# Performance work log

Measured on AMD Instinct MI355X. Metric: run time of the kernel, lower is better.

Reference implementation:

```python
import jax, jax.numpy as jnp
import numpy as np

Q_HEADS = 16
KV_HEADS = 4
ROPE_THETA = 10000.0


def _rope(x, seq_len):
    # x: [B, S, H, D]; pairs are consecutive along D (view_as_complex semantics)
    D = x.shape[-1]
    inv_freq = 1.0 / (ROPE_THETA ** (jnp.arange(0, D, 2, dtype=jnp.float32) / D))
    freqs = jnp.arange(seq_len, dtype=jnp.float32)[:, None] * inv_freq  # [S, D/2]
    cos = jnp.cos(freqs)[None, :, None, :]
    sin = jnp.sin(freqs)[None, :, None, :]
    xr = x.reshape(x.shape[:-1] + (D // 2, 2))
    x0, x1 = xr[..., 0], xr[..., 1]
    out = jnp.stack([x0 * cos - x1 * sin, x0 * sin + x1 * cos], axis=-1)
    return out.reshape(x.shape)


def setup_inputs() -> dict:
    key = jax.random.key(0)
    ks = jax.random.split(key, 6)
    B, S, E = 1, 2048, 2048
    KV_DIM = KV_HEADS * (E // Q_HEADS)  # 512
    scale = 0.02
    return {
        "x": jax.random.normal(ks[0], (B, S, E), dtype=jnp.float32),
        "Wq": jax.random.normal(ks[1], (E, E), dtype=jnp.float32) * scale,
        "Wk": jax.random.normal(ks[2], (KV_DIM, E), dtype=jnp.float32) * scale,
        "Wv": jax.random.normal(ks[3], (KV_DIM, E), dtype=jnp.float32) * scale,
        "Wo": jax.random.normal(ks[4], (E, E), dtype=jnp.float32) * scale,
        "bo": jax.random.normal(ks[5], (E,), dtype=jnp.float32) * scale,
        "cache_keys": jnp.zeros((B, S, KV_HEADS, E // Q_HEADS), dtype=jnp.float32),
        "cache_value": jnp.zeros((B, S, KV_HEADS, E // Q_HEADS), dtype=jnp.float32),
        "start_pos": 0,
    }


def reference(x, Wq, Wk, Wv, Wo, bo, cache_keys, cache_value, start_pos):
    B, S, E = x.shape
    hd = E // Q_HEADS
    G = Q_HEADS // KV_HEADS  # queries per kv head

    xq = (x @ Wq.T).reshape(B, S, Q_HEADS, hd)
    xk = (x @ Wk.T).reshape(B, S, KV_HEADS, hd)
    xv = (x @ Wv.T).reshape(B, S, KV_HEADS, hd)

    # Original applies RoPE with positions 0..seq_len-1 for both q and k
    # (freq tensor is sliced [:seq_len] inside apply_rotry_position_embedding).
    xq = _rope(xq, S)
    xk = _rope(xk, S)

    # cache write at start_pos (static python int)
    cache_keys = jax.lax.dynamic_update_slice(cache_keys, xk, (0, start_pos, 0, 0))
    cache_value = jax.lax.dynamic_update_slice(cache_value, xv, (0, start_pos, 0, 0))
    total = start_pos + S
    k_full = cache_keys[:, :total]   # [B, T, KVH, hd]
    v_full = cache_value[:, :total]

    # repeat_interleave over the head axis == GQA expansion
    k = jnp.repeat(k_full, G, axis=2)  # [B, T, QH, hd]
    v = jnp.repeat(v_full, G, axis=2)

    scores = jnp.einsum("bshd,bthd->bhst", xq, k) / jnp.sqrt(jnp.float32(hd))
    causal = jnp.triu(jnp.ones((S, total), dtype=bool), k=1)  # [S, T]
    scores = jnp.where(causal[None, None, :, :], -jnp.inf, scores)
    weights = jax.nn.softmax(scores, axis=-1)
    out = jnp.einsum("bhst,bthd->bshd", weights, v).reshape(B, S, E)
    # dropout p=0.0 / eval mode -> identity
    return out @ Wo.T + bo
```

## Files before the change

kernel.cpp:

```cpp
#include <hip/hip_runtime.h>
#include <stdint.h>

typedef unsigned short u16;
typedef float  f32x4  __attribute__((ext_vector_type(4)));
typedef __bf16 bf16x8 __attribute__((ext_vector_type(8)));
typedef __bf16 bf16x4 __attribute__((ext_vector_type(4)));
typedef unsigned short u16x8 __attribute__((ext_vector_type(8)));
typedef unsigned short u16x4v __attribute__((ext_vector_type(4)));

#define S_LEN 2048
#define E_DIM 2048
#define HD    128
#define QH    16
#define KVH   4
#define KVD   512
#define NQKV  3072
#define QK_SCALE 0.08838834764831845f

#define AS1 __attribute__((address_space(1)))
#define AS3 __attribute__((address_space(3)))

__device__ __forceinline__ u16 f2bf(float f) {
  union { float f; uint32_t u; } v; v.f = f;
  return (u16)((v.u + 0x7FFFu + ((v.u >> 16) & 1u)) >> 16);
}

__global__ void cast_bf16_kernel(const float* __restrict__ in, u16* __restrict__ out) {
  int i = blockIdx.x * blockDim.x + threadIdx.x;
  float4 f = reinterpret_cast<const float4*>(in)[i];
  u16x4v o;
  o[0] = f2bf(f.x); o[1] = f2bf(f.y); o[2] = f2bf(f.z); o[3] = f2bf(f.w);
  reinterpret_cast<u16x4v*>(out)[i] = o;
}

template<bool BIAS>
__global__ __launch_bounds__(256) void gemm_bt_kernel(
    const u16* __restrict__ A, const u16* __restrict__ B,
    float* __restrict__ C, const float* __restrict__ bias,
    int M, int N, int K)
{
  __shared__ u16 As[2][128 * 64];
  __shared__ u16 Bs[2][128 * 64];

  const int tid  = threadIdx.x;
  const int lane = tid & 63;
  const int wid  = tid >> 6;
  const int wr   = (wid >> 1) * 64;
  const int wc   = (wid & 1) * 64;
  const int lr   = lane & 15;
  const int kg   = lane >> 4;

  const int bm = blockIdx.y * 128;
  const int bn = blockIdx.x * 128;

  f32x4 acc[4][4];
  #pragma unroll
  for (int r = 0; r < 4; ++r)
    #pragma unroll
    for (int c = 0; c < 4; ++c) acc[r][c] = (f32x4){0.f, 0.f, 0.f, 0.f};

  const int l8 = lane & 7;
  const int l3 = lane >> 3;
  const int schunk = l8 ^ l3;

  const u16* gA = A + (size_t)(bm + wid*32 + l3) * K + schunk * 8;
  const u16* gB = B + (size_t)(bn + wid*32 + l3) * K + schunk * 8;

  const int sw = lr & 7;

  auto stage = [&](int buf, int kt) {
    #pragma unroll
    for (int i = 0; i < 4; ++i) {
      __builtin_amdgcn_global_load_lds(
          (const AS1 void*)(gA + (size_t)i * 8 * K + kt),
          (AS3 void*)(&As[buf][wid*32*64 + i*8*64]), 16, 0, 0);
      __builtin_amdgcn_global_load_lds(
          (const AS1 void*)(gB + (size_t)i * 8 * K + kt),
          (AS3 void*)(&Bs[buf][wid*32*64 + i*8*64]), 16, 0, 0);
    }
  };

  stage(0, 0);
  __syncthreads();

  int cur = 0;
  for (int kt = 0; kt < K; kt += 64) {
    if (kt + 64 < K) stage(cur ^ 1, kt + 64);
    #pragma unroll
    for (int kk = 0; kk < 2; ++kk) {
      bf16x8 af[4], bfr[4];
      #pragma unroll
      for (int r = 0; r < 4; ++r)
        af[r] = *reinterpret_cast<const bf16x8*>(
            &As[cur][(wr + r*16 + lr)*64 + ((kk*4 + kg) ^ sw)*8]);
      #pragma unroll
      for (int c = 0; c < 4; ++c)
        bfr[c] = *reinterpret_cast<const bf16x8*>(
            &Bs[cur][(wc + c*16 + lr)*64 + ((kk*4 + kg) ^ sw)*8]);
      #pragma unroll
      for (int r = 0; r < 4; ++r)
        #pragma unroll
        for (int c = 0; c < 4; ++c)
          acc[r][c] = __builtin_amdgcn_mfma_f32_16x16x32_bf16(af[r], bfr[c], acc[r][c], 0, 0, 0);
    }
    __syncthreads();
    cur ^= 1;
  }

  const int crow = kg * 4;
  #pragma unroll
  for (int r = 0; r < 4; ++r) {
    #pragma unroll
    for (int c = 0; c < 4; ++c) {
      int gr = bm + wr + r*16 + crow;
      int gc = bn + wc + c*16 + lr;
      float badd = BIAS ? bias[gc] : 0.0f;
      #pragma unroll
      for (int reg = 0; reg < 4; ++reg)
        C[(size_t)(gr + reg)*N + gc] = acc[r][c][reg] + badd;
    }
  }
}

__global__ void rope_split_kernel(const float* __restrict__ qkv,
                                  u16* __restrict__ qb, u16* __restrict__ kb) {
  int idx = blockIdx.x * blockDim.x + threadIdx.x;
  int s  = idx / 1280;
  int cp = idx - s * 1280;
  int col = cp * 2;
  const float* src = qkv + (size_t)s * NQKV + col;
  float x0 = src[0], x1 = src[1];
  int p = (col & 127) >> 1;
  float inv = exp2f((float)p * (-13.287712379549449f / 64.0f));
  float ang = (float)s * inv;
  float sn, cs;
  sincosf(ang, &sn, &cs);
  float o0 = x0 * cs - x1 * sn;
  float o1 = x0 * sn + x1 * cs;
  if (col < E_DIM) {
    o0 *= QK_SCALE; o1 *= QK_SCALE;
    qb[(size_t)s * E_DIM + col]     = f2bf(o0);
    qb[(size_t)s * E_DIM + col + 1] = f2bf(o1);
  } else {
    kb[(size_t)s * KVD + (col - E_DIM)]     = f2bf(o0);
    kb[(size_t)s * KVD + (col - E_DIM) + 1] = f2bf(o1);
  }
}

__global__ void transpose_v_kernel(const float* __restrict__ qkv, u16* __restrict__ vT) {
  __shared__ float tile[32][33];
  const int sbase = blockIdx.x * 32;
  const int cbase = blockIdx.y * 32;
  const int tx = threadIdx.x;
  const int ty = threadIdx.y;
  #pragma unroll
  for (int i = 0; i < 32; i += 8)
    tile[ty + i][tx] = qkv[(size_t)(sbase + ty + i) * NQKV + (E_DIM + KVD) + cbase + tx];
  __syncthreads();
  #pragma unroll
  for (int i = 0; i < 32; i += 8)
    vT[(size_t)(cbase + ty + i) * S_LEN + sbase + tx] = f2bf(tile[tx][ty + i]);
}

__device__ __forceinline__ void attn_tile(
    int t, int qt, int wid, int lr, int kg,
    const bf16x8* qf, f32x4* o, float& mr, float& ls,
    const u16* ks, const u16* vts, u16* ps)
{
  const int sw = lr & 7;
  f32x4 st[4];
  #pragma unroll
  for (int c = 0; c < 4; ++c) st[c] = (f32x4){0.f, 0.f, 0.f, 0.f};
  __builtin_amdgcn_s_setprio(1);
  #pragma unroll
  for (int kk = 0; kk < 4; ++kk) {
    #pragma unroll
    for (int c = 0; c < 4; ++c) {
      bf16x8 kfr = *reinterpret_cast<const bf16x8*>(
          &ks[(c*16 + lr)*128 + ((kk*4 + kg) ^ sw)*8]);
      st[c] = __builtin_amdgcn_mfma_f32_16x16x32_bf16(kfr, qf[kk], st[c], 0, 0, 0);
    }
  }
  __builtin_amdgcn_s_setprio(0);
  if (t == qt) {
    #pragma unroll
    for (int c = 0; c < 4; ++c)
      #pragma unroll
      for (int reg = 0; reg < 4; ++reg)
        if (c*16 + kg*4 + reg > wid*16 + lr) st[c][reg] = -1e30f;
  }
  float cm[4];
  #pragma unroll
  for (int c = 0; c < 4; ++c)
    cm[c] = fmaxf(fmaxf(st[c][0], st[c][1]), fmaxf(st[c][2], st[c][3]));
  float pm = fmaxf(fmaxf(cm[0], cm[1]), fmaxf(cm[2], cm[3]));
  pm = fmaxf(pm, __shfl_xor(pm, 16));
  pm = fmaxf(pm, __shfl_xor(pm, 32));

  if (!__all(pm - mr <= 8.0f)) {
    float nm = fmaxf(mr, pm);
    float alpha = __expf(mr - nm);
    ls *= alpha;
    mr = nm;
    float ar[4];
    #pragma unroll
    for (int reg = 0; reg < 4; ++reg)
      ar[reg] = __shfl(alpha, kg*4 + reg);
    #pragma unroll
    for (int d = 0; d < 8; ++d)
      #pragma unroll
      for (int reg = 0; reg < 4; ++reg)
        o[d][reg] *= ar[reg];
  }

  float p[4][4];
  float csum[4];
  #pragma unroll
  for (int c = 0; c < 4; ++c) {
    #pragma unroll
    for (int reg = 0; reg < 4; ++reg)
      p[c][reg] = __expf(st[c][reg] - mr);
    csum[c] = (p[c][0] + p[c][1]) + (p[c][2] + p[c][3]);
  }
  float sum = (csum[0] + csum[1]) + (csum[2] + csum[3]);
  sum += __shfl_xor(sum, 16);
  sum += __shfl_xor(sum, 32);
  ls += sum;

  #pragma unroll
  for (int c = 0; c < 4; ++c) {
    bf16x4 pk;
    #pragma unroll
    for (int reg = 0; reg < 4; ++reg) pk[reg] = (__bf16)p[c][reg];
    *reinterpret_cast<bf16x4*>(&ps[lr*72 + c*16 + kg*4]) = pk;
  }
  __builtin_amdgcn_s_setprio(1);
  #pragma unroll
  for (int kk = 0; kk < 2; ++kk) {
    bf16x8 pa = *reinterpret_cast<const bf16x8*>(&ps[lr*72 + kk*32 + kg*8]);
    #pragma unroll
    for (int d = 0; d < 8; ++d) {
      bf16x8 vb = *reinterpret_cast<const bf16x8*>(
          &vts[(d*16 + lr)*64 + ((kk*4 + kg) ^ sw)*8]);
      o[d] = __builtin_amdgcn_mfma_f32_16x16x32_bf16(pa, vb, o[d], 0, 0, 0);
    }
  }
  __builtin_amdgcn_s_setprio(0);
}

__global__ __launch_bounds__(256, 2) void attn_kernel(
    const u16* __restrict__ Q, const u16* __restrict__ Kc,
    const u16* __restrict__ VT, u16* __restrict__ Out)
{
  __shared__ u16 Ks[2][64 * 128];
  __shared__ u16 VTs[2][128 * 64];
  __shared__ u16 Ps[4][16 * 72];

  const int x = blockIdx.x;
  int qt, h;
  if (x < 256) { qt = x & 31; h = x >> 5; }
  else         { int xp = x - 256; qt = 31 - (xp & 31); h = 8 + (xp >> 5); }
  const int kvh = h >> 2;
  const int tid  = threadIdx.x;
  const int lane = tid & 63;
  const int wid  = tid >> 6;
  const int lr   = lane & 15;
  const int kg   = lane >> 4;

  const int NT = qt + 1;

  bf16x8 qf[4];
  {
    const u16* qa = Q + (size_t)(qt*64 + wid*16 + lr) * E_DIM + h * HD + kg * 8;
    #pragma unroll
    for (int kk = 0; kk < 4; ++kk)
      qf[kk] = *reinterpret_cast<const bf16x8*>(qa + kk * 32);
  }

  f32x4 o[8];
  #pragma unroll
  for (int d = 0; d < 8; ++d) o[d] = (f32x4){0.f,0.f,0.f,0.f};
  float mr = -1e30f, ls = 0.f;

  u16x8 kreg[4], vreg[4];
  const u16* kbase = Kc + kvh * HD;
  const u16* vbase = VT + (size_t)(kvh * HD) * S_LEN;

  auto stage_load = [&](int t) {
    #pragma unroll
    for (int i = 0; i < 4; ++i) {
      int c = i * 256 + tid;
      kreg[i] = *reinterpret_cast<const u16x8*>(
          kbase + (size_t)(t*64 + (c >> 4)) * KVD + (c & 15) * 8);
      vreg[i] = *reinterpret_cast<const u16x8*>(
          vbase + (size_t)(c >> 3) * S_LEN + t*64 + (c & 7) * 8);
    }
  };
  auto stage_write = [&](int b) {
    #pragma unroll
    for (int i = 0; i < 4; ++i) {
      int c = i * 256 + tid;
      int kr = c >> 4, kc = c & 15;
      *reinterpret_cast<u16x8*>(&Ks[b][kr*128 + (kc ^ (kr & 7))*8]) = kreg[i];
      int vr = c >> 3, vc = c & 7;
      *reinterpret_cast<u16x8*>(&VTs[b][vr*64 + (vc ^ (vr & 7))*8]) = vreg[i];
    }
  };

  int p = 0;
  stage_load(0);
  stage_write(0);
  __syncthreads();

  for (int t = 0; t < NT; ++t) {
    if (t + 1 < NT) stage_load(t + 1);
    attn_tile(t, qt, wid, lr, kg, qf, o, mr, ls, Ks[p], VTs[p], Ps[wid]);
    if (t + 1 < NT) {
      stage_write(p ^ 1);
      __syncthreads();
      p ^= 1;
    }
  }

  {
    float inv = 1.0f / ls;
    float ivq[4];
    #pragma unroll
    for (int reg = 0; reg < 4; ++reg)
      ivq[reg] = __shfl(inv, kg*4 + reg);
    #pragma unroll
    for (int reg = 0; reg < 4; ++reg) {
      int grow = qt*64 + wid*16 + kg*4 + reg;
      #pragma unroll
      for (int d = 0; d < 8; ++d)
        Out[(size_t)grow * E_DIM + h * HD + d*16 + lr] =
            __builtin_bit_cast(u16, (__bf16)(o[d][reg] * ivq[reg]));
    }
  }
}

extern "C" void kernel_launch(void* const* d_in, const int* in_sizes, int n_in,
                              void* d_out, int out_size, void* d_ws, size_t ws_size,
                              hipStream_t stream)
{
  const float* x  = (const float*)d_in[0];
  const float* Wq = (const float*)d_in[1];
  const float* Wk = (const float*)d_in[2];
  const float* Wv = (const float*)d_in[3];
  const float* Wo = (const float*)d_in[4];
  const float* bo = (const float*)d_in[5];
  float* out = (float*)d_out;

  char* w = (char*)d_ws;
  u16*   xb   = (u16*)(w);
  u16*   Wcat = (u16*)(w + (8u  << 20));
  u16*   Wob  = (u16*)(w + (20u << 20));
  float* qkv  = (float*)(w + (28u << 20));
  u16*   qb   = (u16*)(w + (52u << 20));
  u16*   kb   = (u16*)(w + (60u << 20));
  u16*   vT   = (u16*)(w + (62u << 20));
  u16*   attn = (u16*)(w + (64u << 20));
  (void)ws_size; (void)in_sizes; (void)n_in; (void)out_size;

  cast_bf16_kernel<<<4096, 256, 0, stream>>>(x,  xb);
  cast_bf16_kernel<<<4096, 256, 0, stream>>>(Wq, Wcat);
  cast_bf16_kernel<<<1024, 256, 0, stream>>>(Wk, Wcat + (size_t)E_DIM * E_DIM);
  cast_bf16_kernel<<<1024, 256, 0, stream>>>(Wv, Wcat + (size_t)(E_DIM + KVD) * E_DIM);
  cast_bf16_kernel<<<4096, 256, 0, stream>>>(Wo, Wob);

  gemm_bt_kernel<false><<<dim3(NQKV/128, S_LEN/128), 256, 0, stream>>>(
      xb, Wcat, qkv, nullptr, S_LEN, NQKV, E_DIM);

  rope_split_kernel<<<(S_LEN * 1280) / 256, 256, 0, stream>>>(qkv, qb, kb);
  transpose_v_kernel<<<dim3(S_LEN/32, KVD/32), dim3(32, 8), 0, stream>>>(qkv, vT);

  attn_kernel<<<512, 256, 0, stream>>>(qb, kb, vT, attn);

  gemm_bt_kernel<true><<<dim3(E_DIM/128, S_LEN/128), 256, 0, stream>>>(
      attn, Wob, out, bo, S_LEN, E_DIM, E_DIM);
}
```

Baseline: 153.6 us.

## Stream V from global directly, DMA K to LDS, raise occupancy

The attention kernel drops the V shared-memory staging and reads V^T fragments straight from global memory into registers for the PV MFMAs. K tiles are now copied with global_load_lds direct-to-LDS DMA, which removes the register round trip and the separate LDS write step. The swizzle moves to the source address. Freeing LDS lets the launch bound go from 2 to 3 blocks per CU, and the block-to-(qt,h) mapping is reshuffled to pair short and long causal rows. The risk is that V global reads sit on the critical path with higher latency, and that there are more redundant L2 reads across the four q-heads sharing each KV head.

```diff
diff --git a/kernel.cpp b/kernel.cpp
--- a/kernel.cpp
+++ b/kernel.cpp
@@ -165,7 +165,7 @@
 __device__ __forceinline__ void attn_tile(
     int t, int qt, int wid, int lr, int kg,
     const bf16x8* qf, f32x4* o, float& mr, float& ls,
-    const u16* ks, const u16* vts, u16* ps)
+    const u16* ks, const u16* vcol, u16* ps)
 {
   const int sw = lr & 7;
   f32x4 st[4];
@@ -234,33 +234,46 @@
     for (int reg = 0; reg < 4; ++reg) pk[reg] = (__bf16)p[c][reg];
     *reinterpret_cast<bf16x4*>(&ps[lr*72 + c*16 + kg*4]) = pk;
   }
-  __builtin_amdgcn_s_setprio(1);
-  #pragma unroll
-  for (int kk = 0; kk < 2; ++kk) {
-    bf16x8 pa = *reinterpret_cast<const bf16x8*>(&ps[lr*72 + kk*32 + kg*8]);
-    #pragma unroll
-    for (int d = 0; d < 8; ++d) {
-      bf16x8 vb = *reinterpret_cast<const bf16x8*>(
-          &vts[(d*16 + lr)*64 + ((kk*4 + kg) ^ sw)*8]);
-      o[d] = __builtin_amdgcn_mfma_f32_16x16x32_bf16(pa, vb, o[d], 0, 0, 0);
-    }
-  }
-  __builtin_amdgcn_s_setprio(0);
-}
-
-__global__ __launch_bounds__(256, 2) void attn_kernel(
+
+  bf16x8 pa[2];
+  #pragma unroll
+  for (int kk = 0; kk < 2; ++kk)
+    pa[kk] = *reinterpret_cast<const bf16x8*>(&ps[lr*72 + kk*32 + kg*8]);
+  #pragma unroll
+  for (int half = 0; half < 2; ++half) {
+    bf16x8 vb[4][2];
+    #pragma unroll
+    for (int d0 = 0; d0 < 4; ++d0)
+      #pragma unroll
+      for (int kk = 0; kk < 2; ++kk)
+        vb[d0][kk] = *reinterpret_cast<const bf16x8*>(
+            vcol + (size_t)((half*4 + d0)*16 + lr) * S_LEN + kk*32 + kg*8);
+    __builtin_amdgcn_s_setprio(1);
+    #pragma unroll
+    for (int d0 = 0; d0 < 4; ++d0)
+      #pragma unroll
+      for (int kk = 0; kk < 2; ++kk)
+        o[half*4 + d0] = __builtin_amdgcn_mfma_f32_16x16x32_bf16(
+            pa[kk], vb[d0][kk], o[half*4 + d0], 0, 0, 0);
+    __builtin_amdgcn_s_setprio(0);
+  }
+}
+
+__global__ __launch_bounds__(256, 3) void attn_kernel(
     const u16* __restrict__ Q, const u16* __restrict__ Kc,
     const u16* __restrict__ VT, u16* __restrict__ Out)
 {
   __shared__ u16 Ks[2][64 * 128];
-  __shared__ u16 VTs[2][128 * 64];
   __shared__ u16 Ps[4][16 * 72];
 
-  const int x = blockIdx.x;
-  int qt, h;
-  if (x < 256) { qt = x & 31; h = x >> 5; }
-  else         { int xp = x - 256; qt = 31 - (xp & 31); h = 8 + (xp >> 5); }
-  const int kvh = h >> 2;
+  const int x    = blockIdx.x;
+  const int pp   = x >> 1;
+  const int base = pp & 15;
+  const int h    = (pp >> 4) & 15;
+  const int flip = (x ^ (x >> 8)) & 1;
+  const int qt   = flip ? 31 - base : base;
+  const int kvh  = h >> 2;
+
   const int tid  = threadIdx.x;
   const int lane = tid & 63;
   const int wid  = tid >> 6;
@@ -282,41 +295,30 @@
   for (int d = 0; d < 8; ++d) o[d] = (f32x4){0.f,0.f,0.f,0.f};
   float mr = -1e30f, ls = 0.f;
 
-  u16x8 kreg[4], vreg[4];
   const u16* kbase = Kc + kvh * HD;
   const u16* vbase = VT + (size_t)(kvh * HD) * S_LEN;
 
-  auto stage_load = [&](int t) {
-    #pragma unroll
-    for (int i = 0; i < 4; ++i) {
-      int c = i * 256 + tid;
-      kreg[i] = *reinterpret_cast<const u16x8*>(
-          kbase + (size_t)(t*64 + (c >> 4)) * KVD + (c & 15) * 8);
-      vreg[i] = *reinterpret_cast<const u16x8*>(
-          vbase + (size_t)(c >> 3) * S_LEN + t*64 + (c & 7) * 8);
+  const int krow_off = lane >> 4;
+  const int kchunk   = lane & 15;
+  auto k_dma = [&](int buf, int t) {
+    #pragma unroll
+    for (int j = 0; j < 4; ++j) {
+      int r = j*16 + wid*4 + krow_off;
+      const u16* src = kbase + (size_t)(t*64 + r) * KVD + ((kchunk ^ (r & 7)) * 8);
+      __builtin_amdgcn_global_load_lds(
+          (const AS1 void*)src,
+          (AS3 void*)(&Ks[buf][(j*16 + wid*4) * 128]), 16, 0, 0);
     }
   };
-  auto stage_write = [&](int b) {
-    #pragma unroll
-    for (int i = 0; i < 4; ++i) {
-      int c = i * 256 + tid;
-      int kr = c >> 4, kc = c & 15;
-      *reinterpret_cast<u16x8*>(&Ks[b][kr*128 + (kc ^ (kr & 7))*8]) = kreg[i];
-      int vr = c >> 3, vc = c & 7;
-      *reinterpret_cast<u16x8*>(&VTs[b][vr*64 + (vc ^ (vr & 7))*8]) = vreg[i];
-    }
-  };
+
+  k_dma(0, 0);
+  __syncthreads();
 
   int p = 0;
-  stage_load(0);
-  stage_write(0);
-  __syncthreads();
-
   for (int t = 0; t < NT; ++t) {
-    if (t + 1 < NT) stage_load(t + 1);
-    attn_tile(t, qt, wid, lr, kg, qf, o, mr, ls, Ks[p], VTs[p], Ps[wid]);
+    if (t + 1 < NT) k_dma(p ^ 1, t + 1);
+    attn_tile(t, qt, wid, lr, kg, qf, o, mr, ls, Ks[p], vbase + t*64, Ps[wid]);
     if (t + 1 < NT) {
-      stage_write(p ^ 1);
       __syncthreads();
       p ^= 1;
     }
```

Result: slower. 202.5 us (+31.9%).
